# Kernel optimization log

Measured on AMD Instinct MI355X. Metric: run time of the kernel, lower is better.

## Reference

```python
import jax, jax.numpy as jnp
import numpy as np

B, CIN, COUT, H, W = 2, 128, 128, 128, 256
KH, KW = 3, 3
CMID = 32  # COUT // low_factor


def setup_inputs() -> dict:
    key = jax.random.key(0)
    ks = jax.random.split(key, 7)
    x = jax.random.normal(ks[0], (B, CIN, H, W), jnp.float32)
    # torchvision deform_conv2d offset layout: [2*KH*KW, Ho, Wo], (dy, dx) per tap
    offset = jax.random.normal(ks[1], (2 * KH * KW, H, W), jnp.float32)
    weight = jax.random.normal(ks[2], (COUT, CIN, KH, KW), jnp.float32) * 0.05
    bias = jax.random.normal(ks[3], (COUT,), jnp.float32) * 0.01
    down_w = jax.random.normal(ks[4], (CMID, 2 * COUT), jnp.float32) * 0.05
    up_w = jax.random.normal(ks[5], (COUT, CMID), jnp.float32) * 0.05
    scale = jnp.float32(1.0)
    return dict(x=x, offset=offset, weight=weight, bias=bias,
                down_w=down_w, up_w=up_w, scale=scale)


def _deform_conv2d(x, offset, weight, bias):
    # stride=1, padding=1, dilation=1, groups=1 (matches init_conv config)
    Bn, C, Hh, Ww = x.shape
    Co, _, kh, kw = weight.shape
    K = kh * kw
    Ho, Wo = offset.shape[-2:]
    off = offset.reshape(K, 2, Ho, Wo)
    dy, dx = off[:, 0], off[:, 1]                      # [K, Ho, Wo]
    ki, kj = jnp.meshgrid(jnp.arange(kh), jnp.arange(kw), indexing='ij')
    ki = ki.reshape(K).astype(jnp.float32)
    kj = kj.reshape(K).astype(jnp.float32)
    i = jnp.arange(Ho, dtype=jnp.float32)
    j = jnp.arange(Wo, dtype=jnp.float32)
    PAD = 1.0
    py = i[None, :, None] - PAD + ki[:, None, None] + dy   # [K, Ho, Wo]
    px = j[None, None, :] - PAD + kj[:, None, None] + dx
    y0 = jnp.floor(py).astype(jnp.int32)
    x0 = jnp.floor(px).astype(jnp.int32)
    fy = py - y0.astype(py.dtype)
    fx = px - x0.astype(px.dtype)
    xf = x.reshape(Bn, C, Hh * Ww)

    def gather(yi, xi, w):
        # zero padding outside the image (torchvision semantics)
        valid = (yi >= 0) & (yi < Hh) & (xi >= 0) & (xi < Ww)
        yc = jnp.clip(yi, 0, Hh - 1)
        xc = jnp.clip(xi, 0, Ww - 1)
        idx = (yc * Ww + xc).reshape(-1)                   # [K*Ho*Wo]
        g = xf[:, :, idx].reshape(Bn, C, K, Ho, Wo)
        return g * (w * valid.astype(w.dtype))[None, None]

    val = gather(y0, x0, (1.0 - fy) * (1.0 - fx))
    val = val + gather(y0, x0 + 1, (1.0 - fy) * fx)
    val = val + gather(y0 + 1, x0, fy * (1.0 - fx))
    val = val + gather(y0 + 1, x0 + 1, fy * fx)
    out = jnp.einsum('bcnij,ocn->boij', val, weight.reshape(Co, C, K))
    return out + bias[None, :, None, None]


def reference(x, offset, weight, bias, down_w, up_w, scale):
    # h = original frozen conv (weights shared with the deform branch, ablation != wo_copy)
    h = jax.lax.conv_general_dilated(
        x, weight, window_strides=(1, 1), padding=[(1, 1), (1, 1)],
        dimension_numbers=('NCHW', 'OIHW', 'NCHW'))
    h = h + bias[None, :, None, None]
    dx = _deform_conv2d(x, offset, weight, bias)
    dx = jnp.concatenate([dx, h], axis=1)                  # mix == 'cat'
    lo = jnp.einsum('bcij,dc->bdij', dx, down_w)           # 1x1 conv_down
    up = jnp.einsum('bcij,dc->bdij', lo, up_w)             # 1x1 conv_up
    return h + scale * up
```

## Files before the change

### kernel.cpp

```cpp
#include <hip/hip_runtime.h>
#include <hip/hip_bf16.h>

typedef __attribute__((ext_vector_type(8))) short short8;
typedef __attribute__((ext_vector_type(8))) unsigned short ushort8;
typedef __attribute__((ext_vector_type(4))) float f32x4;
typedef __attribute__((ext_vector_type(4))) int int4v;
typedef __attribute__((ext_vector_type(4))) float float4v;
typedef __attribute__((ext_vector_type(2))) float float2v;
typedef __attribute__((ext_vector_type(4))) unsigned int uint4v;

#define HH 128
#define WW 256
#define CIN_ 128
#define COUT_ 128

__device__ __forceinline__ float bf2f(unsigned short u) {
  return __builtin_bit_cast(float, ((unsigned int)u) << 16);
}
__device__ __forceinline__ unsigned short f2bf(float f) {
  union { __hip_bfloat16 h; unsigned short u; } v;
  v.h = __float2bfloat16(f);
  return v.u;
}

__global__ void k_prep_T(const float* __restrict__ down_w,
                         const float* __restrict__ weight,
                         float* __restrict__ T) {
  int e = blockIdx.x * 256 + threadIdx.x;
  if (e >= 2 * 32 * 1152) return;
  int s = e / 36864, r = e % 36864, d = r / 1152, ck = r % 1152;
  float a = 0.f;
  #pragma unroll 4
  for (int p = 0; p < 128; ++p)
    a += down_w[d * 256 + s * 128 + p] * weight[p * 1152 + ck];
  T[e] = a;
}

__global__ void k_prep_W(const float* __restrict__ up_w,
                         const float* __restrict__ weight,
                         const float* __restrict__ T,
                         const float* __restrict__ scale,
                         unsigned short* __restrict__ wdef,
                         unsigned short* __restrict__ wstd) {
  int e = blockIdx.x * 256 + threadIdx.x;
  if (e >= 2 * 9 * 128 * 128) return;
  int s = e / 147456, r = e % 147456;
  int tap = r / 16384, o = (r / 128) % 128, c = r % 128;
  int ck = c * 9 + tap;
  const float* Ts = T + s * 36864;
  float a = 0.f;
  #pragma unroll
  for (int d = 0; d < 32; ++d) a += up_w[o * 32 + d] * Ts[d * 1152 + ck];
  float scl = scale[0];
  int idx = ((tap * 4 + (c >> 5)) * 128 + o) * 32 + (c & 31);
  if (s == 1) {
    wstd[idx] = f2bf(weight[o * 1152 + ck] + scl * a);
  } else {
    wdef[idx] = f2bf(scl * a);
  }
}

__global__ void k_prep_bias(const float* __restrict__ down_w,
                            const float* __restrict__ up_w,
                            const float* __restrict__ bias,
                            const float* __restrict__ scale,
                            float* __restrict__ beff) {
  __shared__ float sd[32];
  int t = threadIdx.x;
  if (t < 32) {
    float a = 0.f;
    for (int p = 0; p < 128; ++p)
      a += (down_w[t * 256 + p] + down_w[t * 256 + 128 + p]) * bias[p];
    sd[t] = a;
  }
  __syncthreads();
  if (t < 128) {
    float a = 0.f;
    #pragma unroll
    for (int d = 0; d < 32; ++d) a += up_w[t * 32 + d] * sd[d];
    beff[t] = bias[t] + scale[0] * a;
  }
}

__global__ __launch_bounds__(256) void k_nhwc(const float* __restrict__ x,
                                              unsigned short* __restrict__ xh) {
  __shared__ float tile[32 * 129];
  int idx = blockIdx.x;
  int b = idx >> 10, rem = idx & 1023;
  int y = rem >> 3, xg = (rem & 7) << 5;
  int tid = threadIdx.x;
  for (int it = tid; it < 32 * 128; it += 256) {
    int c = it >> 5, xi = it & 31;
    tile[xi * 129 + c] = x[(((size_t)b * 128 + c) * 128 + y) * 256 + xg + xi];
  }
  __syncthreads();
  for (int it = tid; it < 32 * 16; it += 256) {
    int xi = it >> 4, cs = it & 15;
    ushort8 v;
    #pragma unroll
    for (int e = 0; e < 8; ++e) v[e] = f2bf(tile[xi * 129 + cs * 8 + e]);
    *(ushort8*)(xh + (((size_t)b * 128 + y) * 256 + xg + xi) * 128 + cs * 8) = v;
  }
}

__global__ void k_meta(const float* __restrict__ offset,
                       int4v* __restrict__ mo, float4v* __restrict__ mw) {
  int e = blockIdx.x * 256 + threadIdx.x;
  if (e >= 9 * 128 * 256) return;
  int k = e >> 15, rem = e & 32767;
  int ii = rem >> 8, jj = rem & 255;
  float dy = offset[(2 * k) * 32768 + rem];
  float dx = offset[(2 * k + 1) * 32768 + rem];
  int ki = k / 3, kj = k % 3;
  float py = (float)(ii - 1 + ki) + dy;
  float px = (float)(jj - 1 + kj) + dx;
  float fy0 = floorf(py), fx0 = floorf(px);
  int y0 = (int)fy0, x0 = (int)fx0;
  float fy = py - fy0, fx = px - fx0;
  int ys[2] = {y0, y0 + 1};
  int xs_[2] = {x0, x0 + 1};
  float wy[2] = {1.f - fy, fy}, wx[2] = {1.f - fx, fx};
  int4v o;
  float4v w;
  #pragma unroll
  for (int cy = 0; cy < 2; ++cy) {
    #pragma unroll
    for (int cx = 0; cx < 2; ++cx) {
      int yy = ys[cy], xx = xs_[cx];
      bool valid = (yy >= 0) && (yy < HH) && (xx < WW) && (xx >= 0);
      int yc = min(max(yy, 0), HH - 1), xc = min(max(xx, 0), WW - 1);
      int off = (yc * WW + xc) * CIN_;
      float wv = valid ? wy[cy] * wx[cx] : 0.f;
      int ci = cy * 2 + cx;
      if (ci == 0) { o.x = off; w.x = wv; }
      else if (ci == 1) { o.y = off; w.y = wv; }
      else if (ci == 2) { o.z = off; w.z = wv; }
      else { o.w = off; w.w = wv; }
    }
  }
  mo[e] = o;
  mw[e] = w;
}

__global__ __launch_bounds__(256, 4) void k_main(
    const unsigned short* __restrict__ xh,
    const int4v* __restrict__ mo, const float4v* __restrict__ mw,
    const unsigned short* __restrict__ wstd, const unsigned short* __restrict__ wdef,
    const float* __restrict__ beff, float* __restrict__ out) {
  __shared__ __align__(16) unsigned short sbuf[2][64 * 128];

  int orig = blockIdx.x;
  int t = ((orig & 7) << 7) + (orig >> 3);
  int b = t >> 9, i = (t >> 2) & 127, j0 = (t & 3) << 6;
  int tid = threadIdx.x;
  const unsigned short* xb = xh + (size_t)b * (HH * WW * CIN_);

  int slot = tid & 15, pg = tid >> 4;
  int ce = slot * 8;

  int lane = tid & 63, wid = tid >> 6;
  int obase = wid << 5;
  int lrow = lane & 15, lhi = lane >> 4;

  f32x4 acc[2][4] = {};

  auto STAGE_DEF = [&](int tap, unsigned short* buf) {
    int4v o;
    float4v wq0, wq1;
    uint4v g0[4], g1[4];
    int mbase = (tap * HH + i) * WW + j0 + pg;

    o = mo[mbase]; wq0 = mw[mbase];
    g0[0] = *(const uint4v*)(xb + o.x + ce);
    g0[1] = *(const uint4v*)(xb + o.y + ce);
    g0[2] = *(const uint4v*)(xb + o.z + ce);
    g0[3] = *(const uint4v*)(xb + o.w + ce);
    o = mo[mbase + 16]; wq1 = mw[mbase + 16];
    g1[0] = *(const uint4v*)(xb + o.x + ce);
    g1[1] = *(const uint4v*)(xb + o.y + ce);
    g1[2] = *(const uint4v*)(xb + o.z + ce);
    g1[3] = *(const uint4v*)(xb + o.w + ce);

    auto COMB = [&](uint4v* g, float4v w, int q) {
      int p = q * 16 + pg;
      uint4v r;
      #pragma unroll
      for (int wi = 0; wi < 4; ++wi) {
        unsigned u0 = g[0][wi], u1 = g[1][wi], u2 = g[2][wi], u3 = g[3][wi];
        float2v f0 = {__builtin_bit_cast(float, u0 << 16), __builtin_bit_cast(float, u0 & 0xffff0000u)};
        float2v f1 = {__builtin_bit_cast(float, u1 << 16), __builtin_bit_cast(float, u1 & 0xffff0000u)};
        float2v f2 = {__builtin_bit_cast(float, u2 << 16), __builtin_bit_cast(float, u2 & 0xffff0000u)};
        float2v f3 = {__builtin_bit_cast(float, u3 << 16), __builtin_bit_cast(float, u3 & 0xffff0000u)};
        float2v s = w.x * f0 + w.y * f1 + w.z * f2 + w.w * f3;
        r[wi] = (unsigned)f2bf(s.x) | ((unsigned)f2bf(s.y) << 16);
      }
      *(uint4v*)((char*)buf + (p << 8) + ((slot ^ (p & 15)) << 4)) = r;
    };

    COMB(g0, wq0, 0);
    o = mo[mbase + 32]; wq0 = mw[mbase + 32];
    g0[0] = *(const uint4v*)(xb + o.x + ce);
    g0[1] = *(const uint4v*)(xb + o.y + ce);
    g0[2] = *(const uint4v*)(xb + o.z + ce);
    g0[3] = *(const uint4v*)(xb + o.w + ce);
    COMB(g1, wq1, 1);
    o = mo[mbase + 48]; wq1 = mw[mbase + 48];
    g1[0] = *(const uint4v*)(xb + o.x + ce);
    g1[1] = *(const uint4v*)(xb + o.y + ce);
    g1[2] = *(const uint4v*)(xb + o.z + ce);
    g1[3] = *(const uint4v*)(xb + o.w + ce);
    COMB(g0, wq0, 2);
    COMB(g1, wq1, 3);
  };

  auto STAGE_STD = [&](int tap, unsigned short* buf) {
    int ki = tap / 3, kj = tap % 3;
    int gy = i - 1 + ki;
    bool oky = (unsigned)gy < (unsigned)HH;
    uint4v s[4];
    #pragma unroll
    for (int q = 0; q < 4; ++q) {
      int p = q * 16 + pg;
      int gx = j0 + p - 1 + kj;
      uint4v vv = {};
      if (oky && (unsigned)gx < (unsigned)WW)
        vv = *(const uint4v*)(xb + (size_t)(gy * WW + gx) * CIN_ + ce);
      s[q] = vv;
    }
    #pragma unroll
    for (int q = 0; q < 4; ++q) {
      int p = q * 16 + pg;
      *(uint4v*)((char*)buf + (p << 8) + ((slot ^ (p & 15)) << 4)) = s[q];
    }
  };

  auto COMPUTE = [&](int v) {
    const unsigned short* cur = sbuf[v & 1];
    const unsigned short* wt = ((v & 1) ? wdef : wstd) + (size_t)(v >> 1) * 16384;
    short8 af[4][2];
    #pragma unroll
    for (int cc = 0; cc < 4; ++cc)
      #pragma unroll
      for (int am = 0; am < 2; ++am)
        af[cc][am] = *(const short8*)(wt + ((size_t)(cc * 128 + obase + am * 16 + lrow)) * 32 + lhi * 8);
    #pragma unroll
    for (int cc = 0; cc < 4; ++cc) {
      short8 bfr[4];
      #pragma unroll
      for (int bn = 0; bn < 4; ++bn) {
        int pp = bn * 16 + lrow;
        bfr[bn] = *(const short8*)((const char*)cur + (pp << 8) +
                                   (((cc * 4 + lhi) ^ lrow) << 4));
      }
      #pragma unroll
      for (int am = 0; am < 2; ++am)
        #pragma unroll
        for (int bn = 0; bn < 4; ++bn)
          acc[am][bn] = __builtin_amdgcn_mfma_f32_16x16x32_bf16(af[cc][am], bfr[bn], acc[am][bn], 0, 0, 0);
    }
  };

  STAGE_STD(0, sbuf[0]);
  __syncthreads();

  for (int v = 0; v < 18; ++v) {
    if (v < 17) {
      int nv = v + 1;
      if (nv & 1) STAGE_DEF(nv >> 1, sbuf[nv & 1]);
      else        STAGE_STD(nv >> 1, sbuf[nv & 1]);
    }
    COMPUTE(v);
    __syncthreads();
  }

  #pragma unroll
  for (int am = 0; am < 2; ++am) {
    #pragma unroll
    for (int bn = 0; bn < 4; ++bn) {
      int jg = j0 + bn * 16 + lrow;
      #pragma unroll
      for (int r = 0; r < 4; ++r) {
        int o = obase + am * 16 + lhi * 4 + r;
        out[(((size_t)b * COUT_ + o) * HH + i) * WW + jg] = acc[am][bn][r] + beff[o];
      }
    }
  }
}

extern "C" void kernel_launch(void* const* d_in, const int* in_sizes, int n_in,
                              void* d_out, int out_size, void* d_ws, size_t ws_size,
                              hipStream_t stream) {
  const float* x      = (const float*)d_in[0];
  const float* offset = (const float*)d_in[1];
  const float* weight = (const float*)d_in[2];
  const float* bias   = (const float*)d_in[3];
  const float* down_w = (const float*)d_in[4];
  const float* up_w   = (const float*)d_in[5];
  const float* scale  = (const float*)d_in[6];
  float* out = (float*)d_out;

  char* ws = (char*)d_ws;
  unsigned short* xh   = (unsigned short*)(ws);
  int4v* mo            = (int4v*)(ws + 16777216);
  float4v* mw          = (float4v*)(ws + 21495808);
  unsigned short* wstd = (unsigned short*)(ws + 26214400);
  unsigned short* wdef = (unsigned short*)(ws + 26509312);
  float* T             = (float*)(ws + 26804224);
  float* beff          = (float*)(ws + 27099136);

  k_prep_T<<<dim3(288), dim3(256), 0, stream>>>(down_w, weight, T);
  k_prep_W<<<dim3(1152), dim3(256), 0, stream>>>(up_w, weight, T, scale, wdef, wstd);
  k_prep_bias<<<dim3(1), dim3(128), 0, stream>>>(down_w, up_w, bias, scale, beff);
  k_nhwc<<<dim3(2048), dim3(256), 0, stream>>>(x, xh);
  k_meta<<<dim3(1152), dim3(256), 0, stream>>>(offset, mo, mw);
  k_main<<<dim3(1024), dim3(256), 0, stream>>>(xh, mo, mw, wstd, wdef, beff, out);
}
```

Baseline: 114.8 us.

## Warp-specialize main kernel into producer/consumer waves and merge prep kernels

The main kernel now launches 512 threads: four producer waves gather and bilinearly combine the deformable and standard im2col tiles into LDS, while four consumer waves run the MFMA GEMM. Both roles step through a matched sequence of block barriers on the double buffer, so staging of the next tap overlaps with compute on the current one. The five preprocessing kernels are merged into two branch-dispatched kernels to cut launch overhead, and the bf16 packing uses v_cvt_pk_bf16_f32 inline asm. The larger block under launch_bounds(512,4) may limit registers and occupancy, and the producer waves sit idle during MFMA work.

Result: faster. 105.2 us (-8.3%).

```diff
diff --git a/kernel.cpp b/kernel.cpp
--- a/kernel.cpp
+++ b/kernel.cpp
@@ -14,135 +14,130 @@
 #define CIN_ 128
 #define COUT_ 128
 
-__device__ __forceinline__ float bf2f(unsigned short u) {
-  return __builtin_bit_cast(float, ((unsigned int)u) << 16);
-}
 __device__ __forceinline__ unsigned short f2bf(float f) {
   union { __hip_bfloat16 h; unsigned short u; } v;
   v.h = __float2bfloat16(f);
   return v.u;
 }
 
-__global__ void k_prep_T(const float* __restrict__ down_w,
-                         const float* __restrict__ weight,
-                         float* __restrict__ T) {
-  int e = blockIdx.x * 256 + threadIdx.x;
-  if (e >= 2 * 32 * 1152) return;
-  int s = e / 36864, r = e % 36864, d = r / 1152, ck = r % 1152;
-  float a = 0.f;
-  #pragma unroll 4
-  for (int p = 0; p < 128; ++p)
-    a += down_w[d * 256 + s * 128 + p] * weight[p * 1152 + ck];
-  T[e] = a;
-}
-
-__global__ void k_prep_W(const float* __restrict__ up_w,
-                         const float* __restrict__ weight,
-                         const float* __restrict__ T,
-                         const float* __restrict__ scale,
-                         unsigned short* __restrict__ wdef,
-                         unsigned short* __restrict__ wstd) {
-  int e = blockIdx.x * 256 + threadIdx.x;
-  if (e >= 2 * 9 * 128 * 128) return;
-  int s = e / 147456, r = e % 147456;
-  int tap = r / 16384, o = (r / 128) % 128, c = r % 128;
-  int ck = c * 9 + tap;
-  const float* Ts = T + s * 36864;
-  float a = 0.f;
-  #pragma unroll
-  for (int d = 0; d < 32; ++d) a += up_w[o * 32 + d] * Ts[d * 1152 + ck];
-  float scl = scale[0];
-  int idx = ((tap * 4 + (c >> 5)) * 128 + o) * 32 + (c & 31);
-  if (s == 1) {
-    wstd[idx] = f2bf(weight[o * 1152 + ck] + scl * a);
+__global__ __launch_bounds__(256) void k_pre1(
+    const float* __restrict__ down_w, const float* __restrict__ weight,
+    float* __restrict__ T,
+    const float* __restrict__ x, unsigned short* __restrict__ xh,
+    const float* __restrict__ offset, int4v* __restrict__ mo,
+    float4v* __restrict__ mw) {
+  __shared__ float tile[32 * 129];
+  int bid = blockIdx.x;
+  int tid = threadIdx.x;
+
+  if (bid < 288) {
+    int e = bid * 256 + tid;
+    if (e >= 2 * 32 * 1152) return;
+    int s = e / 36864, r = e % 36864, d = r / 1152, ck = r % 1152;
+    float a = 0.f;
+    #pragma unroll 4
+    for (int p = 0; p < 128; ++p)
+      a += down_w[d * 256 + s * 128 + p] * weight[p * 1152 + ck];
+    T[e] = a;
+  } else if (bid < 2336) {
+    int idx = bid - 288;
+    int b = idx >> 10, rem = idx & 1023;
+    int y = rem >> 3, xg = (rem & 7) << 5;
+    for (int it = tid; it < 32 * 128; it += 256) {
+      int c = it >> 5, xi = it & 31;
+      tile[xi * 129 + c] = x[(((size_t)b * 128 + c) * 128 + y) * 256 + xg + xi];
+    }
+    __syncthreads();
+    for (int it = tid; it < 32 * 16; it += 256) {
+      int xi = it >> 4, cs = it & 15;
+      ushort8 v;
+      #pragma unroll
+      for (int e = 0; e < 8; ++e) v[e] = f2bf(tile[xi * 129 + cs * 8 + e]);
+      *(ushort8*)(xh + (((size_t)b * 128 + y) * 256 + xg + xi) * 128 + cs * 8) = v;
+    }
   } else {
-    wdef[idx] = f2bf(scl * a);
+    int e = (bid - 2336) * 256 + tid;
+    if (e >= 9 * 128 * 256) return;
+    int k = e >> 15, rem = e & 32767;
+    int ii = rem >> 8, jj = rem & 255;
+    float dy = offset[(2 * k) * 32768 + rem];
+    float dx = offset[(2 * k + 1) * 32768 + rem];
+    int ki = k / 3, kj = k % 3;
+    float py = (float)(ii - 1 + ki) + dy;
+    float px = (float)(jj - 1 + kj) + dx;
+    float fy0 = floorf(py), fx0 = floorf(px);
+    int y0 = (int)fy0, x0 = (int)fx0;
+    float fy = py - fy0, fx = px - fx0;
+    int ys[2] = {y0, y0 + 1};
+    int xs_[2] = {x0, x0 + 1};
+    float wy[2] = {1.f - fy, fy}, wx[2] = {1.f - fx, fx};
+    int4v o;
+    float4v w;
+    #pragma unroll
+    for (int cy = 0; cy < 2; ++cy) {
+      #pragma unroll
+      for (int cx = 0; cx < 2; ++cx) {
+        int yy = ys[cy], xx = xs_[cx];
+        bool valid = (yy >= 0) && (yy < HH) && (xx < WW) && (xx >= 0);
+        int yc = min(max(yy, 0), HH - 1), xc = min(max(xx, 0), WW - 1);
+        int off = (yc * WW + xc) * CIN_;
+        float wv = valid ? wy[cy] * wx[cx] : 0.f;
+        int ci = cy * 2 + cx;
+        if (ci == 0) { o.x = off; w.x = wv; }
+        else if (ci == 1) { o.y = off; w.y = wv; }
+        else if (ci == 2) { o.z = off; w.z = wv; }
+        else { o.w = off; w.w = wv; }
+      }
+    }
+    mo[e] = o;
+    mw[e] = w;
   }
 }
 
-__global__ void k_prep_bias(const float* __restrict__ down_w,
-                            const float* __restrict__ up_w,
-                            const float* __restrict__ bias,
-                            const float* __restrict__ scale,
-                            float* __restrict__ beff) {
+__global__ __launch_bounds__(256) void k_pre2(
+    const float* __restrict__ up_w, const float* __restrict__ weight,
+    const float* __restrict__ T, const float* __restrict__ scale,
+    unsigned short* __restrict__ wdef, unsigned short* __restrict__ wstd,
+    const float* __restrict__ down_w, const float* __restrict__ bias,
+    float* __restrict__ beff) {
   __shared__ float sd[32];
+  int bid = blockIdx.x;
   int t = threadIdx.x;
-  if (t < 32) {
-    float a = 0.f;
-    for (int p = 0; p < 128; ++p)
-      a += (down_w[t * 256 + p] + down_w[t * 256 + 128 + p]) * bias[p];
-    sd[t] = a;
-  }
-  __syncthreads();
-  if (t < 128) {
+  if (bid < 1152) {
+    int e = bid * 256 + t;
+    if (e >= 2 * 9 * 128 * 128) return;
+    int s = e / 147456, r = e % 147456;
+    int tap = r / 16384, o = (r / 128) % 128, c = r % 128;
+    int ck = c * 9 + tap;
+    const float* Ts = T + s * 36864;
     float a = 0.f;
     #pragma unroll
-    for (int d = 0; d < 32; ++d) a += up_w[t * 32 + d] * sd[d];
-    beff[t] = bias[t] + scale[0] * a;
+    for (int d = 0; d < 32; ++d) a += up_w[o * 32 + d] * Ts[d * 1152 + ck];
+    float scl = scale[0];
+    int idx = ((tap * 4 + (c >> 5)) * 128 + o) * 32 + (c & 31);
+    if (s == 1) {
+      wstd[idx] = f2bf(weight[o * 1152 + ck] + scl * a);
+    } else {
+      wdef[idx] = f2bf(scl * a);
+    }
+  } else {
+    if (t < 32) {
+      float a = 0.f;
+      for (int p = 0; p < 128; ++p)
+        a += (down_w[t * 256 + p] + down_w[t * 256 + 128 + p]) * bias[p];
+      sd[t] = a;
+    }
+    __syncthreads();
+    if (t < 128) {
+      float a = 0.f;
+      #pragma unroll
+      for (int d = 0; d < 32; ++d) a += up_w[t * 32 + d] * sd[d];
+      beff[t] = bias[t] + scale[0] * a;
+    }
   }
 }
 
-__global__ __launch_bounds__(256) void k_nhwc(const float* __restrict__ x,
-                                              unsigned short* __restrict__ xh) {
-  __shared__ float tile[32 * 129];
-  int idx = blockIdx.x;
-  int b = idx >> 10, rem = idx & 1023;
-  int y = rem >> 3, xg = (rem & 7) << 5;
-  int tid = threadIdx.x;
-  for (int it = tid; it < 32 * 128; it += 256) {
-    int c = it >> 5, xi = it & 31;
-    tile[xi * 129 + c] = x[(((size_t)b * 128 + c) * 128 + y) * 256 + xg + xi];
-  }
-  __syncthreads();
-  for (int it = tid; it < 32 * 16; it += 256) {
-    int xi = it >> 4, cs = it & 15;
-    ushort8 v;
-    #pragma unroll
-    for (int e = 0; e < 8; ++e) v[e] = f2bf(tile[xi * 129 + cs * 8 + e]);
-    *(ushort8*)(xh + (((size_t)b * 128 + y) * 256 + xg + xi) * 128 + cs * 8) = v;
-  }
-}
-
-__global__ void k_meta(const float* __restrict__ offset,
-                       int4v* __restrict__ mo, float4v* __restrict__ mw) {
-  int e = blockIdx.x * 256 + threadIdx.x;
-  if (e >= 9 * 128 * 256) return;
-  int k = e >> 15, rem = e & 32767;
-  int ii = rem >> 8, jj = rem & 255;
-  float dy = offset[(2 * k) * 32768 + rem];
-  float dx = offset[(2 * k + 1) * 32768 + rem];
-  int ki = k / 3, kj = k % 3;
-  float py = (float)(ii - 1 + ki) + dy;
-  float px = (float)(jj - 1 + kj) + dx;
-  float fy0 = floorf(py), fx0 = floorf(px);
-  int y0 = (int)fy0, x0 = (int)fx0;
-  float fy = py - fy0, fx = px - fx0;
-  int ys[2] = {y0, y0 + 1};
-  int xs_[2] = {x0, x0 + 1};
-  float wy[2] = {1.f - fy, fy}, wx[2] = {1.f - fx, fx};
-  int4v o;
-  float4v w;
-  #pragma unroll
-  for (int cy = 0; cy < 2; ++cy) {
-    #pragma unroll
-    for (int cx = 0; cx < 2; ++cx) {
-      int yy = ys[cy], xx = xs_[cx];
-      bool valid = (yy >= 0) && (yy < HH) && (xx < WW) && (xx >= 0);
-      int yc = min(max(yy, 0), HH - 1), xc = min(max(xx, 0), WW - 1);
-      int off = (yc * WW + xc) * CIN_;
-      float wv = valid ? wy[cy] * wx[cx] : 0.f;
-      int ci = cy * 2 + cx;
-      if (ci == 0) { o.x = off; w.x = wv; }
-      else if (ci == 1) { o.y = off; w.y = wv; }
-      else if (ci == 2) { o.z = off; w.z = wv; }
-      else { o.w = off; w.w = wv; }
-    }
-  }
-  mo[e] = o;
-  mw[e] = w;
-}
-
-__global__ __launch_bounds__(256, 4) void k_main(
+__global__ __launch_bounds__(512, 4) void k_main(
     const unsigned short* __restrict__ xh,
     const int4v* __restrict__ mo, const float4v* __restrict__ mw,
     const unsigned short* __restrict__ wstd, const unsigned short* __restrict__ wdef,
@@ -155,33 +150,15 @@
   int tid = threadIdx.x;
   const unsigned short* xb = xh + (size_t)b * (HH * WW * CIN_);
 
-  int slot = tid & 15, pg = tid >> 4;
-  int ce = slot * 8;
-
-  int lane = tid & 63, wid = tid >> 6;
-  int obase = wid << 5;
-  int lrow = lane & 15, lhi = lane >> 4;
-
-  f32x4 acc[2][4] = {};
-
-  auto STAGE_DEF = [&](int tap, unsigned short* buf) {
-    int4v o;
-    float4v wq0, wq1;
-    uint4v g0[4], g1[4];
-    int mbase = (tap * HH + i) * WW + j0 + pg;
-
-    o = mo[mbase]; wq0 = mw[mbase];
-    g0[0] = *(const uint4v*)(xb + o.x + ce);
-    g0[1] = *(const uint4v*)(xb + o.y + ce);
-    g0[2] = *(const uint4v*)(xb + o.z + ce);
-    g0[3] = *(const uint4v*)(xb + o.w + ce);
-    o = mo[mbase + 16]; wq1 = mw[mbase + 16];
-    g1[0] = *(const uint4v*)(xb + o.x + ce);
-    g1[1] = *(const uint4v*)(xb + o.y + ce);
-    g1[2] = *(const uint4v*)(xb + o.z + ce);
-    g1[3] = *(const uint4v*)(xb + o.w + ce);
-
-    auto COMB = [&](uint4v* g, float4v w, int q) {
+  int wid = tid >> 6;
+  bool producer = wid < 4;
+
+  if (producer) {
+    int ptid = tid;
+    int slot = ptid & 15, pg = ptid >> 4;
+    int ce = slot * 8;
+
+    auto COMB = [&](uint4v* g, float4v w, int q, unsigned short* buf) {
       int p = q * 16 + pg;
       uint4v r;
       #pragma unroll
@@ -192,96 +169,123 @@
         float2v f2 = {__builtin_bit_cast(float, u2 << 16), __builtin_bit_cast(float, u2 & 0xffff0000u)};
         float2v f3 = {__builtin_bit_cast(float, u3 << 16), __builtin_bit_cast(float, u3 & 0xffff0000u)};
         float2v s = w.x * f0 + w.y * f1 + w.z * f2 + w.w * f3;
-        r[wi] = (unsigned)f2bf(s.x) | ((unsigned)f2bf(s.y) << 16);
+        unsigned rr;
+        asm("v_cvt_pk_bf16_f32 %0, %1, %2" : "=v"(rr) : "v"(s.x), "v"(s.y));
+        r[wi] = rr;
       }
       *(uint4v*)((char*)buf + (p << 8) + ((slot ^ (p & 15)) << 4)) = r;
     };
 
-    COMB(g0, wq0, 0);
-    o = mo[mbase + 32]; wq0 = mw[mbase + 32];
-    g0[0] = *(const uint4v*)(xb + o.x + ce);
-    g0[1] = *(const uint4v*)(xb + o.y + ce);
-    g0[2] = *(const uint4v*)(xb + o.z + ce);
-    g0[3] = *(const uint4v*)(xb + o.w + ce);
-    COMB(g1, wq1, 1);
-    o = mo[mbase + 48]; wq1 = mw[mbase + 48];
-    g1[0] = *(const uint4v*)(xb + o.x + ce);
-    g1[1] = *(const uint4v*)(xb + o.y + ce);
-    g1[2] = *(const uint4v*)(xb + o.z + ce);
-    g1[3] = *(const uint4v*)(xb + o.w + ce);
-    COMB(g0, wq0, 2);
-    COMB(g1, wq1, 3);
-  };
-
-  auto STAGE_STD = [&](int tap, unsigned short* buf) {
-    int ki = tap / 3, kj = tap % 3;
-    int gy = i - 1 + ki;
-    bool oky = (unsigned)gy < (unsigned)HH;
-    uint4v s[4];
+    auto STAGE_DEF = [&](int tap, unsigned short* buf) {
+      int4v o;
+      float4v wq0, wq1;
+      uint4v g0[4], g1[4];
+      int mbase = (tap * HH + i) * WW + j0 + pg;
+
+      o = mo[mbase]; wq0 = mw[mbase];
+      g0[0] = *(const uint4v*)(xb + o.x + ce);
+      g0[1] = *(const uint4v*)(xb + o.y + ce);
+      g0[2] = *(const uint4v*)(xb + o.z + ce);
+      g0[3] = *(const uint4v*)(xb + o.w + ce);
+      o = mo[mbase + 16]; wq1 = mw[mbase + 16];
+      g1[0] = *(const uint4v*)(xb + o.x + ce);
+      g1[1] = *(const uint4v*)(xb + o.y + ce);
+      g1[2] = *(const uint4v*)(xb + o.z + ce);
+      g1[3] = *(const uint4v*)(xb + o.w + ce);
+
+      COMB(g0, wq0, 0, buf);
+      o = mo[mbase + 32]; wq0 = mw[mbase + 32];
+      g0[0] = *(const uint4v*)(xb + o.x + ce);
+      g0[1] = *(const uint4v*)(xb + o.y + ce);
+      g0[2] = *(const uint4v*)(xb + o.z + ce);
+      g0[3] = *(const uint4v*)(xb + o.w + ce);
+      COMB(g1, wq1, 1, buf);
+      o = mo[mbase + 48]; wq1 = mw[mbase + 48];
+      g1[0] = *(const uint4v*)(xb + o.x + ce);
+      g1[1] = *(const uint4v*)(xb + o.y + ce);
+      g1[2] = *(const uint4v*)(xb + o.z + ce);
+      g1[3] = *(const uint4v*)(xb + o.w + ce);
+      COMB(g0, wq0, 2, buf);
+      COMB(g1, wq1, 3, buf);
+    };
+
+    auto STAGE_STD = [&](int tap, unsigned short* buf) {
+      int ki = tap / 3, kj = tap % 3;
+      int gy = i - 1 + ki;
+      bool oky = (unsigned)gy < (unsigned)HH;
+      uint4v s[4];
+      #pragma unroll
+      for (int q = 0; q < 4; ++q) {
+        int p = q * 16 + pg;
+        int gx = j0 + p - 1 + kj;
+        uint4v vv = {};
+        if (oky && (unsigned)gx < (unsigned)WW)
+          vv = *(const uint4v*)(xb + (size_t)(gy * WW + gx) * CIN_ + ce);
+        s[q] = vv;
+      }
+      #pragma unroll
+      for (int q = 0; q < 4; ++q) {
+        int p = q * 16 + pg;
+        *(uint4v*)((char*)buf + (p << 8) + ((slot ^ (p & 15)) << 4)) = s[q];
+      }
+    };
+
+    STAGE_STD(0, sbuf[0]);
+    __syncthreads();
+    for (int v = 0; v < 18; ++v) {
+      if (v < 17) {
+        int nv = v + 1;
+        if (nv & 1) STAGE_DEF(nv >> 1, sbuf[nv & 1]);
+        else        STAGE_STD(nv >> 1, sbuf[nv & 1]);
+      }
+      __syncthreads();
+    }
+  } else {
+    int lane = tid & 63;
+    int cw = wid - 4;
+    int obase = cw << 5;
+    int lrow = lane & 15, lhi = lane >> 4;
+
+    f32x4 acc[2][4] = {};
+
+    __syncthreads();
+    for (int v = 0; v < 18; ++v) {
+      const unsigned short* cur = sbuf[v & 1];
+      const unsigned short* wt = ((v & 1) ? wdef : wstd) + (size_t)(v >> 1) * 16384;
+      short8 af[4][2];
+      #pragma unroll
+      for (int cc = 0; cc < 4; ++cc)
+        #pragma unroll
+        for (int am = 0; am < 2; ++am)
+          af[cc][am] = *(const short8*)(wt + ((size_t)(cc * 128 + obase + am * 16 + lrow)) * 32 + lhi * 8);
+      #pragma unroll
+      for (int cc = 0; cc < 4; ++cc) {
+        short8 bfr[4];
+        #pragma unroll
+        for (int bn = 0; bn < 4; ++bn) {
+          int pp = bn * 16 + lrow;
+          bfr[bn] = *(const short8*)((const char*)cur + (pp << 8) +
+                                     (((cc * 4 + lhi) ^ lrow) << 4));
+        }
+        #pragma unroll
+        for (int am = 0; am < 2; ++am)
+          #pragma unroll
+          for (int bn = 0; bn < 4; ++bn)
+            acc[am][bn] = __builtin_amdgcn_mfma_f32_16x16x32_bf16(af[cc][am], bfr[bn], acc[am][bn], 0, 0, 0);
+      }
+      __syncthreads();
+    }
+
     #pragma unroll
-    for (int q = 0; q < 4; ++q) {
-      int p = q * 16 + pg;
-      int gx = j0 + p - 1 + kj;
-      uint4v vv = {};
-      if (oky && (unsigned)gx < (unsigned)WW)
-        vv = *(const uint4v*)(xb + (size_t)(gy * WW + gx) * CIN_ + ce);
-      s[q] = vv;
-    }
-    #pragma unroll
-    for (int q = 0; q < 4; ++q) {
-      int p = q * 16 + pg;
-      *(uint4v*)((char*)buf + (p << 8) + ((slot ^ (p & 15)) << 4)) = s[q];
-    }
-  };
-
-  auto COMPUTE = [&](int v) {
-    const unsigned short* cur = sbuf[v & 1];
-    const unsigned short* wt = ((v & 1) ? wdef : wstd) + (size_t)(v >> 1) * 16384;
-    short8 af[4][2];
-    #pragma unroll
-    for (int cc = 0; cc < 4; ++cc)
-      #pragma unroll
-      for (int am = 0; am < 2; ++am)
-        af[cc][am] = *(const short8*)(wt + ((size_t)(cc * 128 + obase + am * 16 + lrow)) * 32 + lhi * 8);
-    #pragma unroll
-    for (int cc = 0; cc < 4; ++cc) {
-      short8 bfr[4];
+    for (int am = 0; am < 2; ++am) {
       #pragma unroll
       for (int bn = 0; bn < 4; ++bn) {
-        int pp = bn * 16 + lrow;
-        bfr[bn] = *(const short8*)((const char*)cur + (pp << 8) +
-                                   (((cc * 4 + lhi) ^ lrow) << 4));
-      }
-      #pragma unroll
-      for (int am = 0; am < 2; ++am)
+        int jg = j0 + bn * 16 + lrow;
         #pragma unroll
-        for (int bn = 0; bn < 4; ++bn)
-          acc[am][bn] = __builtin_amdgcn_mfma_f32_16x16x32_bf16(af[cc][am], bfr[bn], acc[am][bn], 0, 0, 0);
-    }
-  };
-
-  STAGE_STD(0, sbuf[0]);
-  __syncthreads();
-
-  for (int v = 0; v < 18; ++v) {
-    if (v < 17) {
-      int nv = v + 1;
-      if (nv & 1) STAGE_DEF(nv >> 1, sbuf[nv & 1]);
-      else        STAGE_STD(nv >> 1, sbuf[nv & 1]);
-    }
-    COMPUTE(v);
-    __syncthreads();
-  }
-
-  #pragma unroll
-  for (int am = 0; am < 2; ++am) {
-    #pragma unroll
-    for (int bn = 0; bn < 4; ++bn) {
-      int jg = j0 + bn * 16 + lrow;
-      #pragma unroll
-      for (int r = 0; r < 4; ++r) {
-        int o = obase + am * 16 + lhi * 4 + r;
-        out[(((size_t)b * COUT_ + o) * HH + i) * WW + jg] = acc[am][bn][r] + beff[o];
+        for (int r = 0; r < 4; ++r) {
+          int o = obase + am * 16 + lhi * 4 + r;
+          out[(((size_t)b * COUT_ + o) * HH + i) * WW + jg] = acc[am][bn][r] + beff[o];
+        }
       }
     }
   }
@@ -308,10 +312,7 @@
   float* T             = (float*)(ws + 26804224);
   float* beff          = (float*)(ws + 27099136);
 
-  k_prep_T<<<dim3(288), dim3(256), 0, stream>>>(down_w, weight, T);
-  k_prep_W<<<dim3(1152), dim3(256), 0, stream>>>(up_w, weight, T, scale, wdef, wstd);
-  k_prep_bias<<<dim3(1), dim3(128), 0, stream>>>(down_w, up_w, bias, scale, beff);
-  k_nhwc<<<dim3(2048), dim3(256), 0, stream>>>(x, xh);
-  k_meta<<<dim3(1152), dim3(256), 0, stream>>>(offset, mo, mw);
-  k_main<<<dim3(1024), dim3(256), 0, stream>>>(xh, mo, mw, wstd, wdef, beff, out);
-}
+  k_pre1<<<dim3(3488), dim3(256), 0, stream>>>(down_w, weight, T, x, xh, offset, mo, mw);
+  k_pre2<<<dim3(1153), dim3(256), 0, stream>>>(up_w, weight, T, scale, wdef, wstd, down_w, bias, beff);
+  k_main<<<dim3(1024), dim3(512), 0, stream>>>(xh, mo, mw, wstd, wdef, beff, out);
+}
```
